# Performance work log

Measured on AMD Instinct MI355X. Metric: run time of the kernel, lower is better.

The kernel has to match this reference:

```python
import jax, jax.numpy as jnp
import numpy as np

NUM_CLASSES = 50000
NUM_SAMPLED = 1000
D_MODEL = 1024
BATCH, SEQ = 32, 512


def _log_expected_count(ids, num_sampled, num_classes):
    # TF log-uniform candidate sampler (unique=True):
    # P(c) = log((c+2)/(c+1)) / log(num_classes+1)
    # E[count] = -expm1(num_sampled * log1p(-P))
    ids_f = ids.astype(jnp.float32)
    p = (jnp.log(ids_f + 2.0) - jnp.log(ids_f + 1.0)) / np.float32(np.log(num_classes + 1.0))
    return jnp.log(-jnp.expm1(num_sampled * jnp.log1p(-p)))


def setup_inputs() -> dict:
    key = jax.random.key(0)
    k1, k2, k3, k4 = jax.random.split(key, 4)
    lstm_outputs = jax.random.normal(k1, (BATCH, SEQ, D_MODEL), dtype=jnp.float32)
    next_token_ids = jax.random.randint(k2, (BATCH, SEQ), 0, NUM_CLASSES)
    sampled_ids = jax.random.randint(k3, (BATCH, NUM_SAMPLED), 0, NUM_CLASSES)
    W = jax.random.normal(k4, (NUM_CLASSES, D_MODEL), dtype=jnp.float32) * (1.0 / np.sqrt(D_MODEL))
    b = jnp.zeros((NUM_CLASSES,), dtype=jnp.float32)
    return {"lstm_outputs": lstm_outputs, "next_token_ids": next_token_ids,
            "sampled_ids": sampled_ids, "W": W, "b": b}


def reference(lstm_outputs, next_token_ids, sampled_ids, W, b):
    # Vectorized sampled-softmax loss (tf.nn.sampled_softmax_loss with
    # log-uniform sampler, partition_strategy irrelevant, accidental-hit removal),
    # mapped over the batch dim as the original tf.map_fn does.
    log_q_true = _log_expected_count(next_token_ids, NUM_SAMPLED, NUM_CLASSES)   # [B,T]
    log_q_samp = _log_expected_count(sampled_ids, NUM_SAMPLED, NUM_CLASSES)      # [B,S]

    w_true = W[next_token_ids]                                                   # [B,T,D]
    true_logit = (jnp.einsum('btd,btd->bt', lstm_outputs, w_true)
                  + b[next_token_ids] - log_q_true)                              # [B,T]

    w_samp = W[sampled_ids]                                                      # [B,S,D]
    samp_logits = (jnp.einsum('btd,bsd->bts', lstm_outputs, w_samp)
                   + b[sampled_ids][:, None, :] - log_q_samp[:, None, :])        # [B,T,S]

    # remove accidental hits (sampled id == true label)
    hit = sampled_ids[:, None, :] == next_token_ids[:, :, None]                  # [B,T,S]
    samp_logits = jnp.where(hit, jnp.float32(-1e9), samp_logits)

    all_logits = jnp.concatenate([true_logit[..., None], samp_logits], axis=-1)  # [B,T,1+S]
    # softmax CE with true class at index 0
    losses = jax.nn.logsumexp(all_logits, axis=-1) - true_logit                  # [B,T]
    return 0.5 * jnp.mean(losses)
```

## Files before the change

### kernel.cpp

```cpp
#include <hip/hip_runtime.h>
#include <hip/hip_bf16.h>
#include <cmath>

#define BATCH 32
#define SEQLEN 512
#define NSAMP 1000
#define DMODEL 1024
#define NCHUNK 4

typedef __bf16 bf16x8_t __attribute__((ext_vector_type(8)));
typedef float f32x4_t __attribute__((ext_vector_type(4)));

__device__ __forceinline__ unsigned pack_bf2(float lo, float hi) {
    unsigned ulo = __float_as_uint(lo);
    unsigned uhi = __float_as_uint(hi);
    ulo = (ulo + 0x7fffu + ((ulo >> 16) & 1u)) >> 16;
    uhi = (uhi + 0x7fffu + ((uhi >> 16) & 1u)) & 0xffff0000u;
    return (ulo & 0xffffu) | uhi;
}

__device__ __forceinline__ float log_expected_count(int id) {
    float idf = (float)id;
    float p = log1pf(1.0f / (idf + 1.0f)) * 0.09242316f;
    return logf(-expm1f(1000.0f * log1pf(-p)));
}

#define STAGE(dst, f1, f2)                                                     \
    do {                                                                       \
        uint4 _u;                                                              \
        _u.x = pack_bf2((f1).x, (f1).y);                                       \
        _u.y = pack_bf2((f1).z, (f1).w);                                       \
        _u.z = pack_bf2((f2).x, (f2).y);                                       \
        _u.w = pack_bf2((f2).z, (f2).w);                                       \
        *(uint4*)(dst) = _u;                                                   \
    } while (0)

__global__ __launch_bounds__(256) void prep_kernel(
    const float* __restrict__ h, const int* __restrict__ labels,
    const int* __restrict__ sids, const float* __restrict__ W,
    const float* __restrict__ bias, unsigned short* __restrict__ Wb,
    float* __restrict__ adjw, float* __restrict__ tlw)
{
    const int w = threadIdx.x >> 6, lane = threadIdx.x & 63;
    if (blockIdx.x < 8000) {
        const int row = blockIdx.x * 4 + w;
        const int sv = sids[row];
        const float4* src = (const float4*)(W + (size_t)sv * DMODEL);
        unsigned short* dst = Wb + (size_t)row * DMODEL;
#pragma unroll
        for (int j = 0; j < 4; ++j) {
            float4 v = src[lane + j * 64];
            uint2 u;
            u.x = pack_bf2(v.x, v.y);
            u.y = pack_bf2(v.z, v.w);
            *(uint2*)(dst + (lane + j * 64) * 4) = u;
        }
        if (lane == 0) adjw[row] = bias[sv] - log_expected_count(sv);
    } else {
        const int r = (blockIdx.x - 8000) * 4 + w;
        const int lab = labels[r];
        const float4* hp = (const float4*)(h + (size_t)r * DMODEL);
        const float4* wp = (const float4*)(W + (size_t)lab * DMODEL);
        float s = 0.0f;
#pragma unroll
        for (int j = 0; j < 4; ++j) {
            float4 a = hp[lane + j * 64];
            float4 c = wp[lane + j * 64];
            s += a.x * c.x + a.y * c.y + a.z * c.z + a.w * c.w;
        }
#pragma unroll
        for (int off = 32; off > 0; off >>= 1) s += __shfl_xor(s, off, 64);
        if (lane == 0) tlw[r] = s + bias[lab] - log_expected_count(lab);
    }
}

__global__ __launch_bounds__(256) void sampled_softmax_main(
    const float* __restrict__ h, const int* __restrict__ labels,
    const int* __restrict__ sids, const unsigned short* __restrict__ Wb,
    const float* __restrict__ adjw,
    float* __restrict__ pm, float* __restrict__ pl)
{
    __shared__ __align__(16) unsigned short Albuf[2][64 * 32];
    __shared__ __align__(16) unsigned short Blbuf[2][64 * 32];
    __shared__ float logits[64 * 67];
    __shared__ int   tid_lds[64];
    __shared__ int   sid_lds[64];
    __shared__ float adj_lds[64];
    __shared__ float mpart[4][64];
    __shared__ float lpart[4][64];

    const int tile_t = blockIdx.x;
    const int bb     = blockIdx.y;
    const int chunk  = blockIdx.z;
    const int t0     = tile_t * 64;
    const int tid    = threadIdx.x;
    const int w      = tid >> 6;
    const int lane   = tid & 63;
    const int lm     = lane & 15;
    const int q      = lane >> 4;

    if (tid < 64) tid_lds[tid] = labels[bb * SEQLEN + t0 + tid];

    float m_run = -INFINITY, l_run = 0.0f;

    const int row    = tid >> 2;
    const int cg     = tid & 3;
    const int wchunk = cg ^ (row & 3);
    const int wr = w >> 1, wc = w & 1;
    const int ar0 = 32 * wr + lm;
    const int bc0 = 32 * wc + lm;
    const int achunk = (q ^ (lm & 3)) * 8;
    const float* aG = h + ((size_t)(bb * SEQLEN + t0 + row)) * DMODEL + cg * 8;

    for (int lt = 0; lt < 4; ++lt) {
        const int s0 = (chunk * 4 + lt) * 64;
        const int scount = (NSAMP - s0 < 64) ? (NSAMP - s0) : 64;
        __syncthreads();
        if (tid < 64) {
            const int s = s0 + tid;
            sid_lds[tid] = (s < NSAMP) ? sids[bb * NSAMP + s] : -1;
            adj_lds[tid] = (s < NSAMP) ? adjw[bb * NSAMP + s] : 0.0f;
        }
        int srow = s0 + row;
        if (srow > NSAMP - 1) srow = NSAMP - 1;
        const unsigned short* bG = Wb + (size_t)(bb * NSAMP + srow) * DMODEL + cg * 8;
        __syncthreads();

        f32x4_t acc00 = {0,0,0,0}, acc01 = {0,0,0,0};
        f32x4_t acc10 = {0,0,0,0}, acc11 = {0,0,0,0};

        {
            float4 a1 = *(const float4*)(aG);
            float4 a2 = *(const float4*)(aG + 4);
            uint4  bv = *(const uint4*)(bG);
            STAGE(&Albuf[0][row * 32 + wchunk * 8], a1, a2);
            *(uint4*)&Blbuf[0][row * 32 + wchunk * 8] = bv;
        }
        __syncthreads();

#pragma unroll 2
        for (int kt = 0; kt < 32; ++kt) {
            const int cur = kt & 1;
            float4 a1, a2; uint4 bv;
            const bool more = (kt + 1) < 32;
            if (more) {
                const float* ap = aG + (kt + 1) * 32;
                a1 = *(const float4*)(ap);
                a2 = *(const float4*)(ap + 4);
                bv = *(const uint4*)(bG + (kt + 1) * 32);
            }
            const unsigned short* Ab = Albuf[cur];
            const unsigned short* Bb = Blbuf[cur];
            bf16x8_t fa0 = *(const bf16x8_t*)(Ab + ar0 * 32 + achunk);
            bf16x8_t fa1 = *(const bf16x8_t*)(Ab + (ar0 + 16) * 32 + achunk);
            bf16x8_t fb0 = *(const bf16x8_t*)(Bb + bc0 * 32 + achunk);
            bf16x8_t fb1 = *(const bf16x8_t*)(Bb + (bc0 + 16) * 32 + achunk);
            acc00 = __builtin_amdgcn_mfma_f32_16x16x32_bf16(fa0, fb0, acc00, 0, 0, 0);
            acc01 = __builtin_amdgcn_mfma_f32_16x16x32_bf16(fa0, fb1, acc01, 0, 0, 0);
            acc10 = __builtin_amdgcn_mfma_f32_16x16x32_bf16(fa1, fb0, acc10, 0, 0, 0);
            acc11 = __builtin_amdgcn_mfma_f32_16x16x32_bf16(fa1, fb1, acc11, 0, 0, 0);
            if (more) {
                const int nxt = cur ^ 1;
                STAGE(&Albuf[nxt][row * 32 + wchunk * 8], a1, a2);
                *(uint4*)&Blbuf[nxt][row * 32 + wchunk * 8] = bv;
            }
            __syncthreads();
        }

        {
            f32x4_t accs[2][2] = {{acc00, acc01}, {acc10, acc11}};
#pragma unroll
            for (int ti = 0; ti < 2; ++ti)
#pragma unroll
                for (int si = 0; si < 2; ++si)
#pragma unroll
                    for (int i = 0; i < 4; ++i)
                        logits[(32 * wr + 16 * ti + q * 4 + i) * 67
                               + 32 * wc + 16 * si + lm] = accs[ti][si][i];
        }
        __syncthreads();

        {
            const int r = tid & 63;
            const int labr = tid_lds[r];
            float mloc = -INFINITY, lloc = 0.0f;
#pragma unroll
            for (int j0 = 0; j0 < 16; ++j0) {
                const int j = w * 16 + j0;
                const float x = logits[r * 67 + j] + adj_lds[j];
                const bool valid = (j < scount) && (sid_lds[j] != labr);
                if (valid) {
                    if (x > mloc) { lloc = lloc * __expf(mloc - x) + 1.0f; mloc = x; }
                    else          { lloc += __expf(x - mloc); }
                }
            }
            mpart[w][r] = mloc;
            lpart[w][r] = lloc;
        }
        __syncthreads();
        if (tid < 64) {
#pragma unroll
            for (int p = 0; p < 4; ++p) {
                const float mp = mpart[p][tid];
                const float lp = lpart[p][tid];
                if (lp > 0.0f) {
                    if (mp > m_run) { l_run = l_run * __expf(m_run - mp) + lp; m_run = mp; }
                    else            { l_run += lp * __expf(mp - m_run); }
                }
            }
        }
    }

    if (tid < 64) {
        const int idx = (bb * SEQLEN + t0 + tid) * NCHUNK + chunk;
        pm[idx] = m_run;
        pl[idx] = l_run;
    }
}

__global__ __launch_bounds__(256) void combine_kernel(
    const float* __restrict__ pm, const float* __restrict__ pl,
    const float* __restrict__ tlw, float* __restrict__ bsum)
{
    __shared__ float wsum[4];
    const int tid = threadIdx.x;
    const int w = tid >> 6, lane = tid & 63;
    const int idx = blockIdx.x * 256 + tid;
    float m = -INFINITY, l = 0.0f;
#pragma unroll
    for (int c = 0; c < NCHUNK; ++c) {
        const float mp = pm[idx * NCHUNK + c];
        const float lp = pl[idx * NCHUNK + c];
        if (lp > 0.0f) {
            if (mp > m) { l = l * __expf(m - mp) + lp; m = mp; }
            else        { l += lp * __expf(mp - m); }
        }
    }
    const float t = tlw[idx];
    const float M = fmaxf(m, t);
    float loss = __logf(l * __expf(m - M) + __expf(t - M)) + M - t;
#pragma unroll
    for (int off = 32; off > 0; off >>= 1) loss += __shfl_xor(loss, off, 64);
    if (lane == 0) wsum[w] = loss;
    __syncthreads();
    if (tid == 0) bsum[blockIdx.x] = wsum[0] + wsum[1] + wsum[2] + wsum[3];
}

__global__ void finalize_kernel(const float* __restrict__ bsum, float* __restrict__ out) {
    float v = bsum[threadIdx.x];
#pragma unroll
    for (int off = 32; off > 0; off >>= 1) v += __shfl_xor(v, off, 64);
    if (threadIdx.x == 0) out[0] = v * (0.5f / (float)(BATCH * SEQLEN));
}

extern "C" void kernel_launch(void* const* d_in, const int* in_sizes, int n_in,
                              void* d_out, int out_size, void* d_ws, size_t ws_size,
                              hipStream_t stream) {
    const float* h      = (const float*)d_in[0];
    const int*   labels = (const int*)d_in[1];
    const int*   sids   = (const int*)d_in[2];
    const float* W      = (const float*)d_in[3];
    const float* bias   = (const float*)d_in[4];

    char* base = (char*)d_ws;
    unsigned short* Wb = (unsigned short*)base;
    float* adjw = (float*)(base + 65536000);
    float* tlw  = (float*)(base + 65536000 + 128000);
    float* pmw  = (float*)(base + 65536000 + 128000 + 65536);
    float* plw  = (float*)(base + 65536000 + 128000 + 65536 + 262144);
    float* bsum = (float*)(base + 65536000 + 128000 + 65536 + 262144 + 262144);

    prep_kernel<<<dim3(12096), dim3(256), 0, stream>>>(h, labels, sids, W, bias, Wb, adjw, tlw);
    sampled_softmax_main<<<dim3(8, 32, NCHUNK), dim3(256), 0, stream>>>(
        h, labels, sids, Wb, adjw, pmw, plw);
    combine_kernel<<<dim3(64), dim3(256), 0, stream>>>(pmw, plw, tlw, bsum);
    finalize_kernel<<<dim3(1), dim3(64), 0, stream>>>(bsum, (float*)d_out);
}
```

Measured before the change: 452.3 us.

## Pre-convert activations to bf16 and use 64x256 tiles with direct global-to-LDS loads

The prep kernel now also writes a bf16 copy of the LSTM outputs, so the main kernel no longer reloads fp32 activations and converts them on every sample tile. The main kernel computes a 64x256 logit tile per block with a 4x4 MFMA accumulator grid per wave, which reads the activation tile once instead of four times. Operands are staged through global_load_lds async copies with an XOR swizzle, and the softmax partials are reduced in registers with shuffles instead of through an LDS logits buffer. This costs an extra 32 MB workspace write in prep, more accumulator registers, and a grid reordered to batch-major.

```diff
diff --git a/kernel.cpp b/kernel.cpp
--- a/kernel.cpp
+++ b/kernel.cpp
@@ -1,5 +1,4 @@
 #include <hip/hip_runtime.h>
-#include <hip/hip_bf16.h>
 #include <cmath>
 
 #define BATCH 32
@@ -25,20 +24,18 @@
     return logf(-expm1f(1000.0f * log1pf(-p)));
 }
 
-#define STAGE(dst, f1, f2)                                                     \
-    do {                                                                       \
-        uint4 _u;                                                              \
-        _u.x = pack_bf2((f1).x, (f1).y);                                       \
-        _u.y = pack_bf2((f1).z, (f1).w);                                       \
-        _u.z = pack_bf2((f2).x, (f2).y);                                       \
-        _u.w = pack_bf2((f2).z, (f2).w);                                       \
-        *(uint4*)(dst) = _u;                                                   \
-    } while (0)
+__device__ __forceinline__ void gl16(const void* g, void* l) {
+    __builtin_amdgcn_global_load_lds(
+        (const __attribute__((address_space(1))) unsigned int*)g,
+        (__attribute__((address_space(3))) unsigned int*)l,
+        16, 0, 0);
+}
 
 __global__ __launch_bounds__(256) void prep_kernel(
     const float* __restrict__ h, const int* __restrict__ labels,
     const int* __restrict__ sids, const float* __restrict__ W,
     const float* __restrict__ bias, unsigned short* __restrict__ Wb,
+    unsigned short* __restrict__ hb,
     float* __restrict__ adjw, float* __restrict__ tlw)
 {
     const int w = threadIdx.x >> 6, lane = threadIdx.x & 63;
@@ -61,12 +58,17 @@
         const int lab = labels[r];
         const float4* hp = (const float4*)(h + (size_t)r * DMODEL);
         const float4* wp = (const float4*)(W + (size_t)lab * DMODEL);
+        unsigned short* hdst = hb + (size_t)r * DMODEL;
         float s = 0.0f;
 #pragma unroll
         for (int j = 0; j < 4; ++j) {
             float4 a = hp[lane + j * 64];
             float4 c = wp[lane + j * 64];
             s += a.x * c.x + a.y * c.y + a.z * c.z + a.w * c.w;
+            uint2 u;
+            u.x = pack_bf2(a.x, a.y);
+            u.y = pack_bf2(a.z, a.w);
+            *(uint2*)(hdst + (lane + j * 64) * 4) = u;
         }
 #pragma unroll
         for (int off = 32; off > 0; off >>= 1) s += __shfl_xor(s, off, 64);
@@ -74,147 +76,143 @@
     }
 }
 
-__global__ __launch_bounds__(256) void sampled_softmax_main(
-    const float* __restrict__ h, const int* __restrict__ labels,
-    const int* __restrict__ sids, const unsigned short* __restrict__ Wb,
+__global__ __launch_bounds__(256, 3) void sampled_softmax_main(
+    const int* __restrict__ labels, const int* __restrict__ sids,
+    const unsigned short* __restrict__ hb, const unsigned short* __restrict__ Wb,
     const float* __restrict__ adjw,
     float* __restrict__ pm, float* __restrict__ pl)
 {
-    __shared__ __align__(16) unsigned short Albuf[2][64 * 32];
-    __shared__ __align__(16) unsigned short Blbuf[2][64 * 32];
-    __shared__ float logits[64 * 67];
-    __shared__ int   tid_lds[64];
-    __shared__ int   sid_lds[64];
-    __shared__ float adj_lds[64];
+    __shared__ __align__(16) unsigned short Ab[2][64 * 32];
+    __shared__ __align__(16) unsigned short Bb[2][256 * 32];
+    __shared__ int   sid_lds[256];
+    __shared__ float adj_lds[256];
+    __shared__ int   lab_lds[64];
     __shared__ float mpart[4][64];
     __shared__ float lpart[4][64];
 
-    const int tile_t = blockIdx.x;
-    const int bb     = blockIdx.y;
-    const int chunk  = blockIdx.z;
-    const int t0     = tile_t * 64;
-    const int tid    = threadIdx.x;
-    const int w      = tid >> 6;
-    const int lane   = tid & 63;
-    const int lm     = lane & 15;
-    const int q      = lane >> 4;
-
-    if (tid < 64) tid_lds[tid] = labels[bb * SEQLEN + t0 + tid];
-
-    float m_run = -INFINITY, l_run = 0.0f;
-
-    const int row    = tid >> 2;
-    const int cg     = tid & 3;
-    const int wchunk = cg ^ (row & 3);
-    const int wr = w >> 1, wc = w & 1;
-    const int ar0 = 32 * wr + lm;
-    const int bc0 = 32 * wc + lm;
-    const int achunk = (q ^ (lm & 3)) * 8;
-    const float* aG = h + ((size_t)(bb * SEQLEN + t0 + row)) * DMODEL + cg * 8;
-
-    for (int lt = 0; lt < 4; ++lt) {
-        const int s0 = (chunk * 4 + lt) * 64;
-        const int scount = (NSAMP - s0 < 64) ? (NSAMP - s0) : 64;
+    const int bb     = blockIdx.x;
+    const int chunk  = blockIdx.y;
+    const int tile_t = blockIdx.z;
+    const int t0  = tile_t * 64;
+    const int tid = threadIdx.x;
+    const int w   = tid >> 6, l = tid & 63;
+    const int lm  = l & 15,   q = l >> 4;
+    const int rl4 = l >> 2,  cp = l & 3;
+
+    {
+        const int s = chunk * 256 + tid;
+        const bool v = s < NSAMP;
+        sid_lds[tid] = v ? sids[bb * NSAMP + s] : -1;
+        adj_lds[tid] = v ? adjw[bb * NSAMP + s] : 0.0f;
+        if (tid < 64) lab_lds[tid] = labels[bb * SEQLEN + t0 + tid];
+    }
+
+    const int swzs = (rl4 & 3) ^ ((rl4 >> 2) & 3);
+    const int cs = (cp ^ swzs) * 8;
+    const unsigned short* aS = hb + (size_t)(bb * SEQLEN + t0 + 16 * w + rl4) * DMODEL + cs;
+    const unsigned short* bS[4];
+#pragma unroll
+    for (int j = 0; j < 4; ++j) {
+        int rb = chunk * 256 + 64 * w + 16 * j + rl4;
+        if (rb > NSAMP - 1) rb = NSAMP - 1;
+        bS[j] = Wb + (size_t)(bb * NSAMP + rb) * DMODEL + cs;
+    }
+
+    const int fswz = (lm & 3) ^ ((lm >> 2) & 3);
+    const int fp = (q ^ fswz) * 8;
+    int aoff[4], boff[4];
+#pragma unroll
+    for (int t = 0; t < 4; ++t) aoff[t] = (16 * t + lm) * 32 + fp;
+#pragma unroll
+    for (int c = 0; c < 4; ++c) boff[c] = (64 * w + 16 * c + lm) * 32 + fp;
+
+    f32x4_t acc[4][4];
+#pragma unroll
+    for (int t = 0; t < 4; ++t)
+#pragma unroll
+        for (int c = 0; c < 4; ++c) acc[t][c] = (f32x4_t){0.f, 0.f, 0.f, 0.f};
+
+    gl16(aS, &Ab[0][(16 * w) * 32]);
+#pragma unroll
+    for (int j = 0; j < 4; ++j) gl16(bS[j], &Bb[0][(64 * w + 16 * j) * 32]);
+    __syncthreads();
+
+    for (int kt = 0; kt < 32; ++kt) {
+        const int cur = kt & 1;
+        if (kt + 1 < 32) {
+            const int adv = (kt + 1) * 32;
+            gl16(aS + adv, &Ab[cur ^ 1][(16 * w) * 32]);
+#pragma unroll
+            for (int j = 0; j < 4; ++j)
+                gl16(bS[j] + adv, &Bb[cur ^ 1][(64 * w + 16 * j) * 32]);
+        }
+        const unsigned short* Ac = Ab[cur];
+        const unsigned short* Bc = Bb[cur];
+        bf16x8_t fa[4];
+#pragma unroll
+        for (int t = 0; t < 4; ++t) fa[t] = *(const bf16x8_t*)(Ac + aoff[t]);
+#pragma unroll
+        for (int c = 0; c < 4; ++c) {
+            bf16x8_t fb = *(const bf16x8_t*)(Bc + boff[c]);
+#pragma unroll
+            for (int t = 0; t < 4; ++t)
+                acc[t][c] = __builtin_amdgcn_mfma_f32_16x16x32_bf16(fa[t], fb, acc[t][c], 0, 0, 0);
+        }
         __syncthreads();
-        if (tid < 64) {
-            const int s = s0 + tid;
-            sid_lds[tid] = (s < NSAMP) ? sids[bb * NSAMP + s] : -1;
-            adj_lds[tid] = (s < NSAMP) ? adjw[bb * NSAMP + s] : 0.0f;
-        }
-        int srow = s0 + row;
-        if (srow > NSAMP - 1) srow = NSAMP - 1;
-        const unsigned short* bG = Wb + (size_t)(bb * NSAMP + srow) * DMODEL + cg * 8;
-        __syncthreads();
-
-        f32x4_t acc00 = {0,0,0,0}, acc01 = {0,0,0,0};
-        f32x4_t acc10 = {0,0,0,0}, acc11 = {0,0,0,0};
-
-        {
-            float4 a1 = *(const float4*)(aG);
-            float4 a2 = *(const float4*)(aG + 4);
-            uint4  bv = *(const uint4*)(bG);
-            STAGE(&Albuf[0][row * 32 + wchunk * 8], a1, a2);
-            *(uint4*)&Blbuf[0][row * 32 + wchunk * 8] = bv;
-        }
-        __syncthreads();
-
-#pragma unroll 2
-        for (int kt = 0; kt < 32; ++kt) {
-            const int cur = kt & 1;
-            float4 a1, a2; uint4 bv;
-            const bool more = (kt + 1) < 32;
-            if (more) {
-                const float* ap = aG + (kt + 1) * 32;
-                a1 = *(const float4*)(ap);
-                a2 = *(const float4*)(ap + 4);
-                bv = *(const uint4*)(bG + (kt + 1) * 32);
+    }
+
+    float adjv[4]; int sidv[4]; bool cval[4];
+#pragma unroll
+    for (int c = 0; c < 4; ++c) {
+        const int col = 64 * w + 16 * c + lm;
+        adjv[c] = adj_lds[col];
+        sidv[c] = sid_lds[col];
+        cval[c] = (chunk * 256 + col) < NSAMP;
+    }
+#pragma unroll
+    for (int t = 0; t < 4; ++t) {
+#pragma unroll
+        for (int i = 0; i < 4; ++i) {
+            const int r = 16 * t + 4 * q + i;
+            const int lab = lab_lds[r];
+            float x[4]; bool ok[4];
+            float m = -INFINITY;
+#pragma unroll
+            for (int c = 0; c < 4; ++c) {
+                x[c] = acc[t][c][i] + adjv[c];
+                ok[c] = cval[c] && (sidv[c] != lab);
+                if (ok[c]) m = fmaxf(m, x[c]);
             }
-            const unsigned short* Ab = Albuf[cur];
-            const unsigned short* Bb = Blbuf[cur];
-            bf16x8_t fa0 = *(const bf16x8_t*)(Ab + ar0 * 32 + achunk);
-            bf16x8_t fa1 = *(const bf16x8_t*)(Ab + (ar0 + 16) * 32 + achunk);
-            bf16x8_t fb0 = *(const bf16x8_t*)(Bb + bc0 * 32 + achunk);
-            bf16x8_t fb1 = *(const bf16x8_t*)(Bb + (bc0 + 16) * 32 + achunk);
-            acc00 = __builtin_amdgcn_mfma_f32_16x16x32_bf16(fa0, fb0, acc00, 0, 0, 0);
-            acc01 = __builtin_amdgcn_mfma_f32_16x16x32_bf16(fa0, fb1, acc01, 0, 0, 0);
-            acc10 = __builtin_amdgcn_mfma_f32_16x16x32_bf16(fa1, fb0, acc10, 0, 0, 0);
-            acc11 = __builtin_amdgcn_mfma_f32_16x16x32_bf16(fa1, fb1, acc11, 0, 0, 0);
-            if (more) {
-                const int nxt = cur ^ 1;
-                STAGE(&Albuf[nxt][row * 32 + wchunk * 8], a1, a2);
-                *(uint4*)&Blbuf[nxt][row * 32 + wchunk * 8] = bv;
+            float ls = 0.0f;
+#pragma unroll
+            for (int c = 0; c < 4; ++c) ls += ok[c] ? __expf(x[c] - m) : 0.0f;
+#pragma unroll
+            for (int off = 1; off < 16; off <<= 1) {
+                const float mo = __shfl_xor(m, off, 64);
+                const float lo = __shfl_xor(ls, off, 64);
+                const float M  = fmaxf(m, mo);
+                const float e1 = (ls > 0.0f) ? ls * __expf(m - M) : 0.0f;
+                const float e2 = (lo > 0.0f) ? lo * __expf(mo - M) : 0.0f;
+                m = M; ls = e1 + e2;
             }
-            __syncthreads();
-        }
-
-        {
-            f32x4_t accs[2][2] = {{acc00, acc01}, {acc10, acc11}};
-#pragma unroll
-            for (int ti = 0; ti < 2; ++ti)
-#pragma unroll
-                for (int si = 0; si < 2; ++si)
-#pragma unroll
-                    for (int i = 0; i < 4; ++i)
-                        logits[(32 * wr + 16 * ti + q * 4 + i) * 67
-                               + 32 * wc + 16 * si + lm] = accs[ti][si][i];
-        }
-        __syncthreads();
-
-        {
-            const int r = tid & 63;
-            const int labr = tid_lds[r];
-            float mloc = -INFINITY, lloc = 0.0f;
-#pragma unroll
-            for (int j0 = 0; j0 < 16; ++j0) {
-                const int j = w * 16 + j0;
-                const float x = logits[r * 67 + j] + adj_lds[j];
-                const bool valid = (j < scount) && (sid_lds[j] != labr);
-                if (valid) {
-                    if (x > mloc) { lloc = lloc * __expf(mloc - x) + 1.0f; mloc = x; }
-                    else          { lloc += __expf(x - mloc); }
-                }
+            if (lm == 0) { mpart[w][r] = m; lpart[w][r] = ls; }
+        }
+    }
+    __syncthreads();
+    if (tid < 64) {
+        float m = -INFINITY, lsum = 0.0f;
+#pragma unroll
+        for (int p = 0; p < 4; ++p) {
+            const float mp = mpart[p][tid];
+            const float lp = lpart[p][tid];
+            if (lp > 0.0f) {
+                if (mp > m) { lsum = lsum * __expf(m - mp) + lp; m = mp; }
+                else        { lsum += lp * __expf(mp - m); }
             }
-            mpart[w][r] = mloc;
-            lpart[w][r] = lloc;
-        }
-        __syncthreads();
-        if (tid < 64) {
-#pragma unroll
-            for (int p = 0; p < 4; ++p) {
-                const float mp = mpart[p][tid];
-                const float lp = lpart[p][tid];
-                if (lp > 0.0f) {
-                    if (mp > m_run) { l_run = l_run * __expf(m_run - mp) + lp; m_run = mp; }
-                    else            { l_run += lp * __expf(mp - m_run); }
-                }
-            }
-        }
-    }
-
-    if (tid < 64) {
+        }
         const int idx = (bb * SEQLEN + t0 + tid) * NCHUNK + chunk;
-        pm[idx] = m_run;
-        pl[idx] = l_run;
+        pm[idx] = m;
+        pl[idx] = lsum;
     }
 }
 
@@ -264,15 +262,16 @@
 
     char* base = (char*)d_ws;
     unsigned short* Wb = (unsigned short*)base;
-    float* adjw = (float*)(base + 65536000);
-    float* tlw  = (float*)(base + 65536000 + 128000);
-    float* pmw  = (float*)(base + 65536000 + 128000 + 65536);
-    float* plw  = (float*)(base + 65536000 + 128000 + 65536 + 262144);
-    float* bsum = (float*)(base + 65536000 + 128000 + 65536 + 262144 + 262144);
-
-    prep_kernel<<<dim3(12096), dim3(256), 0, stream>>>(h, labels, sids, W, bias, Wb, adjw, tlw);
-    sampled_softmax_main<<<dim3(8, 32, NCHUNK), dim3(256), 0, stream>>>(
-        h, labels, sids, Wb, adjw, pmw, plw);
+    unsigned short* hb = (unsigned short*)(base + 65536000);
+    float* adjw = (float*)(base + 99090432);
+    float* tlw  = (float*)(base + 99218432);
+    float* pmw  = (float*)(base + 99283968);
+    float* plw  = (float*)(base + 99546112);
+    float* bsum = (float*)(base + 99808256);
+
+    prep_kernel<<<dim3(12096), dim3(256), 0, stream>>>(h, labels, sids, W, bias, Wb, hb, adjw, tlw);
+    sampled_softmax_main<<<dim3(32, NCHUNK, 8), dim3(256), 0, stream>>>(
+        labels, sids, hb, Wb, adjw, pmw, plw);
     combine_kernel<<<dim3(64), dim3(256), 0, stream>>>(pmw, plw, tlw, bsum);
     finalize_kernel<<<dim3(1), dim3(64), 0, stream>>>(bsum, (float*)d_out);
 }
```

Result: faster. 410.2 us (-9.3%).
